# Kernel tuning notes

Measured on AMD Instinct MI355X. Metric: run time of the kernel, lower is better.

Reference implementation:

```python
import jax, jax.numpy as jnp
import numpy as np
from jax import lax

H_STEP = 1.0 / 3.0  # h = (t1 - t0) / N with t0=0, t1=1, N=3
N_STEPS = 3


def _conv(x, w):
    # x: [B, C, H, W], w: [O, I, kh, kw], 'same' padding, stride 1
    return lax.conv_general_dilated(
        x, w, window_strides=(1, 1), padding='SAME',
        dimension_numbers=('NCHW', 'OIHW', 'NCHW'))


def setup_inputs() -> dict:
    key = jax.random.key(0)
    ks = jax.random.split(key, 5)
    B, C, H, W = 16, 128, 128, 128
    fan_in = C * 9
    return {
        'x': jax.random.normal(ks[0], (B, C, H, W), dtype=jnp.float32),
        'w1': jax.random.normal(ks[1], (C, C, 3, 3), dtype=jnp.float32) * (2.0 / fan_in) ** 0.5,
        'b1': jax.random.normal(ks[2], (C,), dtype=jnp.float32) * 0.01,
        'w2': jax.random.normal(ks[3], (C, C, 3, 3), dtype=jnp.float32) * (2.0 / fan_in) ** 0.5,
        'b2': jax.random.normal(ks[4], (C,), dtype=jnp.float32) * 0.01,
    }


def reference(x, w1, b1, w2, b2):
    # Euler-step residual block: x <- x + h * conv2(relu(conv1(x))) for N steps
    for _ in range(N_STEPS):
        t = jax.nn.relu(_conv(x, w1) + b1[None, :, None, None])
        x = x + H_STEP * (_conv(t, w2) + b2[None, :, None, None])
    return jax.nn.relu(x)
```

## Files before the change

### kernel.cpp

```cpp
#include <hip/hip_runtime.h>
#include <hip/hip_bf16.h>


#define BATCH 16
#define CH    128
#define HH    128
#define WW    128
#define H_STEP (1.0f/3.0f)

typedef short bf16x8 __attribute__((ext_vector_type(8)));
typedef float f32x4  __attribute__((ext_vector_type(4)));

__device__ __forceinline__ float bf2f(unsigned short u) {
    union { unsigned int i; float f; } c; c.i = ((unsigned int)u) << 16; return c.f;
}
__device__ __forceinline__ unsigned short f2bf(float f) {
    union { float f; unsigned int i; } c; c.f = f;
    unsigned int i = c.i;
    return (unsigned short)((i + 0x7FFFu + ((i >> 16) & 1u)) >> 16);
}

__device__ __forceinline__ void gload16(const unsigned short* g, unsigned short* l) {
    __builtin_amdgcn_global_load_lds(
        (const __attribute__((address_space(1))) unsigned int*)g,
        (__attribute__((address_space(3))) unsigned int*)l, 16, 0, 0);
}

__global__ __launch_bounds__(256)
void transpose_x(const float* __restrict__ x, unsigned short* __restrict__ xb)
{
    __shared__ unsigned short s[128 * 132];
    const int tid = threadIdx.x;
    const int bz  = blockIdx.x;
    const int b = bz >> 7, y = bz & 127;

    #pragma unroll
    for (int it = 0; it < 16; ++it) {
        int idx = it * 256 + tid;
        int ci = idx >> 5, xq = idx & 31;
        float4 v = *(const float4*)&x[(((size_t)b * CH + ci) * HH + y) * WW + xq * 4];
        uint2 p;
        p.x = (unsigned int)f2bf(v.x) | ((unsigned int)f2bf(v.y) << 16);
        p.y = (unsigned int)f2bf(v.z) | ((unsigned int)f2bf(v.w) << 16);
        *(uint2*)&s[ci * 132 + xq * 4] = p;
    }
    __syncthreads();
    #pragma unroll
    for (int it = 0; it < 8; ++it) {
        int idx = it * 256 + tid;
        int xx = idx >> 4, cc = idx & 15;
        unsigned short t[8];
        #pragma unroll
        for (int k = 0; k < 8; ++k) t[k] = s[(cc * 8 + k) * 132 + xx];
        uint4 p;
        p.x = (unsigned int)t[0] | ((unsigned int)t[1] << 16);
        p.y = (unsigned int)t[2] | ((unsigned int)t[3] << 16);
        p.z = (unsigned int)t[4] | ((unsigned int)t[5] << 16);
        p.w = (unsigned int)t[6] | ((unsigned int)t[7] << 16);
        *(uint4*)&xb[((size_t)(b * HH + y) * WW + xx) * CH + cc * 8] = p;
    }
}

__global__ __launch_bounds__(256)
void convert_w(const float* __restrict__ w, unsigned short* __restrict__ wb)
{
    int idx = blockIdx.x * 256 + threadIdx.x;
    #pragma unroll
    for (int t = 0; t < 9; ++t)
        wb[t * 16384 + idx] = f2bf(w[(size_t)idx * 9 + t]);
}

template<int MODE>
__global__ __launch_bounds__(256, 3)
void conv_mfma(const unsigned short* __restrict__ in,
               const unsigned short* __restrict__ wb,
               const float* __restrict__ bias,
               const unsigned short* resb,
               unsigned short* outb,
               float* __restrict__ outf)
{
    __shared__ unsigned short s_is[2][130 * 32];
    __shared__ unsigned short s_w [3][128 * 32];

    const int tid = threadIdx.x;
    const int bz0 = blockIdx.x;
    const int bz  = ((bz0 & 7) << 8) | (bz0 >> 3);
    const int b = bz >> 7, y = bz & 127;

    const int lane = tid & 63;
    const int wid  = tid >> 6;
    const int woc0 = (wid >> 1) * 64;
    const int wpx0 = (wid & 1) * 64;
    const int n16  = lane & 15;
    const int q    = lane >> 4;

    const int srow = lane >> 2;
    const int slot = lane & 3;

    const int kylo = (y == 0)      ? 1 : 0;
    const int kyhi = (y == HH - 1) ? 1 : 2;
    const int nky  = kyhi - kylo + 1;
    const int NG   = nky * 4;
    const int NS   = NG * 3;

    f32x4 acc[4][4];
    #pragma unroll
    for (int i = 0; i < 4; ++i)
        #pragma unroll
        for (int j = 0; j < 4; ++j) acc[i][j] = (f32x4)0.0f;

    auto stage_w = [&](int tap, int kq, int buf) {
        const unsigned short* wt = wb + tap * 16384 + kq * 32;
        #pragma unroll
        for (int c = 0; c < 2; ++c) {
            int row = (wid * 2 + c) * 16 + srow;
            const unsigned short* src = wt + row * 128 + ((slot ^ (row & 3)) << 3);
            gload16(src, &s_w[buf][(wid * 2 + c) * 512]);
        }
    };
    auto stage_is = [&](int gy, int kq, int buf) {
        const size_t inrow = ((size_t)(b * HH + gy) * WW) * CH + kq * 32;
        #pragma unroll
        for (int c = 0; c < 2; ++c) {
            int r   = (c * 4 + wid) * 16 + srow;
            int swz = (r + 1) & 3;
            const unsigned short* src = in + inrow + (size_t)r * CH + ((slot ^ swz) << 3);
            gload16(src, &s_is[buf][((c * 4 + wid) * 16 + 1) * 32]);
        }
    };

    stage_w(kylo * 3 + 0, 0, 0);
    stage_is(y + kylo - 1, 0, 0);
    stage_w(kylo * 3 + 1, 0, 1);
    if (tid < 16) {
        int bfi = tid >> 3, rr = ((tid >> 2) & 1) ? 129 : 0, cc = tid & 3;
        uint4 z = {0u, 0u, 0u, 0u};
        *(uint4*)&s_is[bfi][rr * 32 + cc * 8] = z;
    }
    asm volatile("s_waitcnt lgkmcnt(0)" ::: "memory");

    const int NSm1 = NS - 1;
    for (int s = 0; s < NS; ++s) {
        const int g   = s / 3;
        const int kx  = s - g * 3;
        const int kyi = g >> 2;
        const int ig  = g & 1;

        if (kx == 0) asm volatile("s_waitcnt vmcnt(2)" ::: "memory");
        else         asm volatile("s_waitcnt vmcnt(4)" ::: "memory");
        asm volatile("s_barrier" ::: "memory");

        {
            int wb2 = (kx == 0) ? 2 : (kx - 1);
            int s2  = s + 2; if (s2 > NSm1) s2 = NSm1;
            int g2  = s2 / 3, kx2 = s2 - g2 * 3;
            stage_w((kylo + (g2 >> 2)) * 3 + kx2, g2 & 3, wb2);
        }
        if (kx == 0) {
            int gn = g + 1; if (gn > NG - 1) gn = NG - 1;
            stage_is(y + kylo + (gn >> 2) - 1, gn & 3, (g + 1) & 1);
        }

        bf16x8 af[4], bfr[4];
        #pragma unroll
        for (int i = 0; i < 4; ++i) {
            int row = woc0 + i * 16 + n16;
            af[i] = *(const bf16x8*)&s_w[kx][row * 32 + ((q ^ (row & 3)) << 3)];
        }
        #pragma unroll
        for (int j = 0; j < 4; ++j) {
            int rowb = wpx0 + j * 16 + n16 + kx;
            bfr[j] = *(const bf16x8*)&s_is[ig][rowb * 32 + ((q ^ (rowb & 3)) << 3)];
        }
        __builtin_amdgcn_s_setprio(1);
        #pragma unroll
        for (int i = 0; i < 4; ++i)
            #pragma unroll
            for (int j = 0; j < 4; ++j)
                acc[i][j] = __builtin_amdgcn_mfma_f32_16x16x32_bf16(
                    af[i], bfr[j], acc[i][j], 0, 0, 0);
        __builtin_amdgcn_s_setprio(0);
    }

    const int ybase = (b * HH + y) * WW;
    if (MODE == 0 || MODE == 1) {
        #pragma unroll
        for (int j = 0; j < 4; ++j) {
            int x = wpx0 + j * 16 + n16;
            size_t pbase = (size_t)(ybase + x) * CH;
            #pragma unroll
            for (int i = 0; i < 4; ++i) {
                int oc0 = woc0 + i * 16 + q * 4;
                float v0 = acc[i][j][0] + bias[oc0 + 0];
                float v1 = acc[i][j][1] + bias[oc0 + 1];
                float v2 = acc[i][j][2] + bias[oc0 + 2];
                float v3 = acc[i][j][3] + bias[oc0 + 3];
                if (MODE == 0) {
                    v0 = fmaxf(v0, 0.f); v1 = fmaxf(v1, 0.f);
                    v2 = fmaxf(v2, 0.f); v3 = fmaxf(v3, 0.f);
                } else {
                    uint2 rr = *(const uint2*)&resb[pbase + oc0];
                    v0 = bf2f((unsigned short)(rr.x & 0xffff)) + H_STEP * v0;
                    v1 = bf2f((unsigned short)(rr.x >> 16))    + H_STEP * v1;
                    v2 = bf2f((unsigned short)(rr.y & 0xffff)) + H_STEP * v2;
                    v3 = bf2f((unsigned short)(rr.y >> 16))    + H_STEP * v3;
                }
                uint2 po;
                po.x = (unsigned int)f2bf(v0) | ((unsigned int)f2bf(v1) << 16);
                po.y = (unsigned int)f2bf(v2) | ((unsigned int)f2bf(v3) << 16);
                *(uint2*)&outb[pbase + oc0] = po;
            }
        }
    } else {
        #pragma unroll
        for (int i = 0; i < 4; ++i) {
            #pragma unroll
            for (int r = 0; r < 4; ++r) {
                int oc = woc0 + i * 16 + q * 4 + r;
                float bv = bias[oc];
                size_t orow = ((size_t)(b * CH + oc) * HH + y) * WW;
                #pragma unroll
                for (int j = 0; j < 4; ++j) {
                    int x = wpx0 + j * 16 + n16;
                    float v = acc[i][j][r] + bv;
                    v = bf2f(resb[(size_t)(ybase + x) * CH + oc]) + H_STEP * v;
                    outf[orow + x] = fmaxf(v, 0.f);
                }
            }
        }
    }
}

extern "C" void kernel_launch(void* const* d_in, const int* in_sizes, int n_in,
                              void* d_out, int out_size, void* d_ws, size_t ws_size,
                              hipStream_t stream) {
    const float* x0 = (const float*)d_in[0];
    const float* w1 = (const float*)d_in[1];
    const float* b1 = (const float*)d_in[2];
    const float* w2 = (const float*)d_in[3];
    const float* b2 = (const float*)d_in[4];

    const size_t NELEM = (size_t)BATCH * CH * HH * WW;
    unsigned short* XB = (unsigned short*)d_ws;
    unsigned short* T  = XB + NELEM;

    unsigned short* WB1;
    if (ws_size >= NELEM * 4 + 2 * 294912)
        WB1 = T + NELEM;
    else
        WB1 = (unsigned short*)d_in[0];
    unsigned short* WB2 = WB1 + 9 * 16384;

    dim3 block(256);
    dim3 gridRow(BATCH * HH);

    transpose_x<<<gridRow, block, 0, stream>>>(x0, XB);
    convert_w<<<dim3(64), block, 0, stream>>>(w1, WB1);
    convert_w<<<dim3(64), block, 0, stream>>>(w2, WB2);

    conv_mfma<0><<<gridRow, block, 0, stream>>>(XB, WB1, b1, nullptr, T, nullptr);
    conv_mfma<1><<<gridRow, block, 0, stream>>>(T, WB2, b2, XB, XB, nullptr);
    conv_mfma<0><<<gridRow, block, 0, stream>>>(XB, WB1, b1, nullptr, T, nullptr);
    conv_mfma<1><<<gridRow, block, 0, stream>>>(T, WB2, b2, XB, XB, nullptr);
    conv_mfma<0><<<gridRow, block, 0, stream>>>(XB, WB1, b1, nullptr, T, nullptr);
    conv_mfma<2><<<gridRow, block, 0, stream>>>(T, WB2, b2, XB, nullptr, (float*)d_out);
}
```

Measured before the change: 823.0 us.

## Use two-wave conv blocks with larger per-wave tiles and LDS-staged epilogue

```diff
diff --git a/kernel.cpp b/kernel.cpp
--- a/kernel.cpp
+++ b/kernel.cpp
@@ -71,7 +71,7 @@
 }
 
 template<int MODE>
-__global__ __launch_bounds__(256, 3)
+__global__ __launch_bounds__(128, 2)
 void conv_mfma(const unsigned short* __restrict__ in,
                const unsigned short* __restrict__ wb,
                const float* __restrict__ bias,
@@ -79,8 +79,9 @@
                unsigned short* outb,
                float* __restrict__ outf)
 {
-    __shared__ unsigned short s_is[2][130 * 32];
-    __shared__ unsigned short s_w [3][128 * 32];
+    __shared__ __align__(16) char smem[41216];
+    unsigned short* s_is = (unsigned short*)smem;
+    unsigned short* s_w  = (unsigned short*)(smem + 16640);
 
     const int tid = threadIdx.x;
     const int bz0 = blockIdx.x;
@@ -89,8 +90,6 @@
 
     const int lane = tid & 63;
     const int wid  = tid >> 6;
-    const int woc0 = (wid >> 1) * 64;
-    const int wpx0 = (wid & 1) * 64;
     const int n16  = lane & 15;
     const int q    = lane >> 4;
 
@@ -103,29 +102,29 @@
     const int NG   = nky * 4;
     const int NS   = NG * 3;
 
-    f32x4 acc[4][4];
+    f32x4 acc[4][8];
     #pragma unroll
     for (int i = 0; i < 4; ++i)
         #pragma unroll
-        for (int j = 0; j < 4; ++j) acc[i][j] = (f32x4)0.0f;
+        for (int j = 0; j < 8; ++j) acc[i][j] = (f32x4)0.0f;
 
     auto stage_w = [&](int tap, int kq, int buf) {
         const unsigned short* wt = wb + tap * 16384 + kq * 32;
         #pragma unroll
-        for (int c = 0; c < 2; ++c) {
-            int row = (wid * 2 + c) * 16 + srow;
+        for (int c = 0; c < 4; ++c) {
+            int row = (wid * 4 + c) * 16 + srow;
             const unsigned short* src = wt + row * 128 + ((slot ^ (row & 3)) << 3);
-            gload16(src, &s_w[buf][(wid * 2 + c) * 512]);
+            gload16(src, s_w + buf * 4096 + (wid * 4 + c) * 512);
         }
     };
     auto stage_is = [&](int gy, int kq, int buf) {
         const size_t inrow = ((size_t)(b * HH + gy) * WW) * CH + kq * 32;
         #pragma unroll
-        for (int c = 0; c < 2; ++c) {
-            int r   = (c * 4 + wid) * 16 + srow;
+        for (int c = 0; c < 4; ++c) {
+            int r   = (wid * 4 + c) * 16 + srow;
             int swz = (r + 1) & 3;
             const unsigned short* src = in + inrow + (size_t)r * CH + ((slot ^ swz) << 3);
-            gload16(src, &s_is[buf][((c * 4 + wid) * 16 + 1) * 32]);
+            gload16(src, s_is + buf * 4160 + ((wid * 4 + c) * 16 + 1) * 32);
         }
     };
 
@@ -135,7 +134,7 @@
     if (tid < 16) {
         int bfi = tid >> 3, rr = ((tid >> 2) & 1) ? 129 : 0, cc = tid & 3;
         uint4 z = {0u, 0u, 0u, 0u};
-        *(uint4*)&s_is[bfi][rr * 32 + cc * 8] = z;
+        *(uint4*)&s_is[bfi * 4160 + rr * 32 + cc * 8] = z;
     }
     asm volatile("s_waitcnt lgkmcnt(0)" ::: "memory");
 
@@ -143,11 +142,10 @@
     for (int s = 0; s < NS; ++s) {
         const int g   = s / 3;
         const int kx  = s - g * 3;
-        const int kyi = g >> 2;
         const int ig  = g & 1;
 
-        if (kx == 0) asm volatile("s_waitcnt vmcnt(2)" ::: "memory");
-        else         asm volatile("s_waitcnt vmcnt(4)" ::: "memory");
+        if (kx == 0) asm volatile("s_waitcnt vmcnt(4)" ::: "memory");
+        else         asm volatile("s_waitcnt vmcnt(8)" ::: "memory");
         asm volatile("s_barrier" ::: "memory");
 
         {
@@ -161,54 +159,100 @@
             stage_is(y + kylo + (gn >> 2) - 1, gn & 3, (g + 1) & 1);
         }
 
-        bf16x8 af[4], bfr[4];
+        bf16x8 af[4], bfr[8];
         #pragma unroll
         for (int i = 0; i < 4; ++i) {
-            int row = woc0 + i * 16 + n16;
-            af[i] = *(const bf16x8*)&s_w[kx][row * 32 + ((q ^ (row & 3)) << 3)];
-        }
-        #pragma unroll
-        for (int j = 0; j < 4; ++j) {
-            int rowb = wpx0 + j * 16 + n16 + kx;
-            bfr[j] = *(const bf16x8*)&s_is[ig][rowb * 32 + ((q ^ (rowb & 3)) << 3)];
+            int row = wid * 64 + i * 16 + n16;
+            af[i] = *(const bf16x8*)&s_w[kx * 4096 + row * 32 + ((q ^ (row & 3)) << 3)];
+        }
+        #pragma unroll
+        for (int j = 0; j < 8; ++j) {
+            int rowb = j * 16 + n16 + kx;
+            bfr[j] = *(const bf16x8*)&s_is[ig * 4160 + rowb * 32 + ((q ^ (rowb & 3)) << 3)];
         }
         __builtin_amdgcn_s_setprio(1);
         #pragma unroll
         for (int i = 0; i < 4; ++i)
             #pragma unroll
-            for (int j = 0; j < 4; ++j)
+            for (int j = 0; j < 8; ++j)
                 acc[i][j] = __builtin_amdgcn_mfma_f32_16x16x32_bf16(
                     af[i], bfr[j], acc[i][j], 0, 0, 0);
         __builtin_amdgcn_s_setprio(0);
     }
 
     const int ybase = (b * HH + y) * WW;
-    if (MODE == 0 || MODE == 1) {
-        #pragma unroll
-        for (int j = 0; j < 4; ++j) {
-            int x = wpx0 + j * 16 + n16;
-            size_t pbase = (size_t)(ybase + x) * CH;
+    if (MODE == 0) {
+        asm volatile("s_waitcnt vmcnt(0) lgkmcnt(0)" ::: "memory");
+        asm volatile("s_barrier" ::: "memory");
+        unsigned short* sep = (unsigned short*)smem;
+        #pragma unroll
+        for (int j = 0; j < 8; ++j) {
+            int px = j * 16 + n16;
+            int sw = (px & 7) << 5;
             #pragma unroll
             for (int i = 0; i < 4; ++i) {
-                int oc0 = woc0 + i * 16 + q * 4;
-                float v0 = acc[i][j][0] + bias[oc0 + 0];
-                float v1 = acc[i][j][1] + bias[oc0 + 1];
-                float v2 = acc[i][j][2] + bias[oc0 + 2];
-                float v3 = acc[i][j][3] + bias[oc0 + 3];
-                if (MODE == 0) {
-                    v0 = fmaxf(v0, 0.f); v1 = fmaxf(v1, 0.f);
-                    v2 = fmaxf(v2, 0.f); v3 = fmaxf(v3, 0.f);
-                } else {
-                    uint2 rr = *(const uint2*)&resb[pbase + oc0];
-                    v0 = bf2f((unsigned short)(rr.x & 0xffff)) + H_STEP * v0;
-                    v1 = bf2f((unsigned short)(rr.x >> 16))    + H_STEP * v1;
-                    v2 = bf2f((unsigned short)(rr.y & 0xffff)) + H_STEP * v2;
-                    v3 = bf2f((unsigned short)(rr.y >> 16))    + H_STEP * v3;
-                }
+                int oc0 = wid * 64 + i * 16 + q * 4;
+                float v0 = fmaxf(acc[i][j][0] + bias[oc0 + 0], 0.f);
+                float v1 = fmaxf(acc[i][j][1] + bias[oc0 + 1], 0.f);
+                float v2 = fmaxf(acc[i][j][2] + bias[oc0 + 2], 0.f);
+                float v3 = fmaxf(acc[i][j][3] + bias[oc0 + 3], 0.f);
                 uint2 po;
                 po.x = (unsigned int)f2bf(v0) | ((unsigned int)f2bf(v1) << 16);
                 po.y = (unsigned int)f2bf(v2) | ((unsigned int)f2bf(v3) << 16);
-                *(uint2*)&outb[pbase + oc0] = po;
+                *(uint2*)((char*)sep + ((px * 256 + oc0 * 2) ^ sw)) = po;
+            }
+        }
+        asm volatile("s_waitcnt lgkmcnt(0)" ::: "memory");
+        asm volatile("s_barrier" ::: "memory");
+        #pragma unroll
+        for (int it = 0; it < 16; ++it) {
+            int idx = it * 128 + tid;
+            int pxr = idx >> 4, cc = idx & 15;
+            uint4 v = *(uint4*)((char*)sep + ((pxr * 256 + cc * 16) ^ ((pxr & 7) << 5)));
+            *(uint4*)&outb[(size_t)(ybase + pxr) * CH + cc * 8] = v;
+        }
+    } else if (MODE == 1) {
+        asm volatile("s_waitcnt vmcnt(0) lgkmcnt(0)" ::: "memory");
+        asm volatile("s_barrier" ::: "memory");
+        float* sf = (float*)smem;
+        #pragma unroll
+        for (int p = 0; p < 2; ++p) {
+            if (p) {
+                asm volatile("s_waitcnt lgkmcnt(0)" ::: "memory");
+                asm volatile("s_barrier" ::: "memory");
+            }
+            #pragma unroll
+            for (int jj = 0; jj < 4; ++jj) {
+                int j   = p * 4 + jj;
+                int pxl = jj * 16 + n16;
+                int sw  = (pxl & 7) << 5;
+                #pragma unroll
+                for (int i = 0; i < 4; ++i) {
+                    int oc0 = wid * 64 + i * 16 + q * 4;
+                    f32x4 w = acc[i][j];
+                    w[0] += bias[oc0 + 0]; w[1] += bias[oc0 + 1];
+                    w[2] += bias[oc0 + 2]; w[3] += bias[oc0 + 3];
+                    *(f32x4*)((char*)sf + ((pxl * 512 + oc0 * 4) ^ sw)) = w;
+                }
+            }
+            asm volatile("s_waitcnt lgkmcnt(0)" ::: "memory");
+            asm volatile("s_barrier" ::: "memory");
+            #pragma unroll
+            for (int it = 0; it < 16; ++it) {
+                int idx = it * 128 + tid;
+                int pxl = idx >> 5, c4 = idx & 31;
+                f32x4 v = *(f32x4*)((char*)sf +
+                            ((pxl * 512 + c4 * 16) ^ ((pxl & 7) << 5)));
+                size_t gb = (size_t)(ybase + p * 64 + pxl) * CH + c4 * 4;
+                uint2 rr = *(const uint2*)&resb[gb];
+                float o0 = bf2f((unsigned short)(rr.x & 0xffff)) + H_STEP * v[0];
+                float o1 = bf2f((unsigned short)(rr.x >> 16))    + H_STEP * v[1];
+                float o2 = bf2f((unsigned short)(rr.y & 0xffff)) + H_STEP * v[2];
+                float o3 = bf2f((unsigned short)(rr.y >> 16))    + H_STEP * v[3];
+                uint2 po;
+                po.x = (unsigned int)f2bf(o0) | ((unsigned int)f2bf(o1) << 16);
+                po.y = (unsigned int)f2bf(o2) | ((unsigned int)f2bf(o3) << 16);
+                *(uint2*)&outb[gb] = po;
             }
         }
     } else {
@@ -216,12 +260,12 @@
         for (int i = 0; i < 4; ++i) {
             #pragma unroll
             for (int r = 0; r < 4; ++r) {
-                int oc = woc0 + i * 16 + q * 4 + r;
+                int oc = wid * 64 + i * 16 + q * 4 + r;
                 float bv = bias[oc];
                 size_t orow = ((size_t)(b * CH + oc) * HH + y) * WW;
                 #pragma unroll
-                for (int j = 0; j < 4; ++j) {
-                    int x = wpx0 + j * 16 + n16;
+                for (int j = 0; j < 8; ++j) {
+                    int x = j * 16 + n16;
                     float v = acc[i][j][r] + bv;
                     v = bf2f(resb[(size_t)(ybase + x) * CH + oc]) + H_STEP * v;
                     outf[orow + x] = fmaxf(v, 0.f);
@@ -252,16 +296,17 @@
     unsigned short* WB2 = WB1 + 9 * 16384;
 
     dim3 block(256);
+    dim3 block2(128);
     dim3 gridRow(BATCH * HH);
 
     transpose_x<<<gridRow, block, 0, stream>>>(x0, XB);
     convert_w<<<dim3(64), block, 0, stream>>>(w1, WB1);
     convert_w<<<dim3(64), block, 0, stream>>>(w2, WB2);
 
-    conv_mfma<0><<<gridRow, block, 0, stream>>>(XB, WB1, b1, nullptr, T, nullptr);
-    conv_mfma<1><<<gridRow, block, 0, stream>>>(T, WB2, b2, XB, XB, nullptr);
-    conv_mfma<0><<<gridRow, block, 0, stream>>>(XB, WB1, b1, nullptr, T, nullptr);
-    conv_mfma<1><<<gridRow, block, 0, stream>>>(T, WB2, b2, XB, XB, nullptr);
-    conv_mfma<0><<<gridRow, block, 0, stream>>>(XB, WB1, b1, nullptr, T, nullptr);
-    conv_mfma<2><<<gridRow, block, 0, stream>>>(T, WB2, b2, XB, nullptr, (float*)d_out);
-}
+    conv_mfma<0><<<gridRow, block2, 0, stream>>>(XB, WB1, b1, nullptr, T, nullptr);
+    conv_mfma<1><<<gridRow, block2, 0, stream>>>(T, WB2, b2, XB, XB, nullptr);
+    conv_mfma<0><<<gridRow, block2, 0, stream>>>(XB, WB1, b1, nullptr, T, nullptr);
+    conv_mfma<1><<<gridRow, block2, 0, stream>>>(T, WB2, b2, XB, XB, nullptr);
+    conv_mfma<0><<<gridRow, block2, 0, stream>>>(XB, WB1, b1, nullptr, T, nullptr);
+    conv_mfma<2><<<gridRow, block2, 0, stream>>>(T, WB2, b2, XB, nullptr, (float*)d_out);
+}
```

Result: slower. 875.1 us (+6.3%).
